# Kernel optimization log

Measured on AMD Instinct MI355X. Metric: run time of the kernel, lower is better.

## Reference

```python
import jax, jax.numpy as jnp
import numpy as np

STATE_DIM = 32
EMBED_DIM = 96
LATENT_DIM = STATE_DIM + EMBED_DIM  # 128
HISTORY = 8
HIST_DIM = HISTORY * STATE_DIM      # 256
CTRL_DIM = 8
HW = 512
BATCH = 4096
HORIZON = 64


def setup_inputs() -> dict:
    key = jax.random.key(0)
    ks = jax.random.split(key, 14)

    def w(k, shape, fan_in):
        return (jax.random.normal(k, shape, jnp.float32) / np.float32(np.sqrt(fan_in)))

    inp = {
        "history_k": jax.random.normal(ks[0], (BATCH, HIST_DIM), jnp.float32),
        "u_seq": jax.random.normal(ks[1], (BATCH, HORIZON, CTRL_DIM), jnp.float32),
        "history_next_seq": jax.random.normal(ks[2], (BATCH, HORIZON, HIST_DIM), jnp.float32),
        # encoder MLP: depth=3 -> 4 linear layers (256->512, 512->512, 512->512, 512->96)
        "enc_W0": w(ks[3], (HW, HIST_DIM), HIST_DIM),
        "enc_b0": jnp.zeros((HW,), jnp.float32),
        "enc_W1": w(ks[4], (HW, HW), HW),
        "enc_b1": jnp.zeros((HW,), jnp.float32),
        "enc_W2": w(ks[5], (HW, HW), HW),
        "enc_b2": jnp.zeros((HW,), jnp.float32),
        "enc_W3": w(ks[6], (EMBED_DIM, HW), HW),
        "enc_b3": jnp.zeros((EMBED_DIM,), jnp.float32),
        # A scaled so spectral radius ~0.9 (stable 64-step rollout)
        "A_W": jax.random.normal(ks[7], (LATENT_DIM, LATENT_DIM), jnp.float32) * np.float32(0.9 / np.sqrt(LATENT_DIM)),
        "B_W": w(ks[8], (LATENT_DIM, CTRL_DIM), CTRL_DIM),
    }
    return inp


def _encoder(x, W0, b0, W1, b1, W2, b2, W3, b3):
    h = jax.nn.relu(x @ W0.T + b0)
    h = jax.nn.relu(h @ W1.T + b1)
    h = jax.nn.relu(h @ W2.T + b2)
    return h @ W3.T + b3


def _lift(hist, W0, b0, W1, b1, W2, b2, W3, b3):
    cur = hist[..., -STATE_DIM:]
    return jnp.concatenate([cur, _encoder(hist, W0, b0, W1, b1, W2, b2, W3, b3)], axis=-1)


def reference(history_k, u_seq, history_next_seq,
              enc_W0, enc_b0, enc_W1, enc_b1, enc_W2, enc_b2, enc_W3, enc_b3,
              A_W, B_W):
    batch, horizon = u_seq.shape[:2]
    z_k = _lift(history_k, enc_W0, enc_b0, enc_W1, enc_b1, enc_W2, enc_b2, enc_W3, enc_b3)  # [B, L]

    hist_flat = history_next_seq.reshape(batch * horizon, HIST_DIM)
    z_target_seq = _lift(hist_flat, enc_W0, enc_b0, enc_W1, enc_b1, enc_W2, enc_b2, enc_W3, enc_b3)
    z_target_seq = z_target_seq.reshape(batch, horizon, LATENT_DIM)

    # Precompute B u_t for all steps: [M, B, L]
    bu = jnp.einsum('bmc,lc->mbl', u_seq, B_W)
    At = A_W.T

    def step(z, bu_t):
        z_next = z @ At + bu_t
        return z_next, z_next

    _, zs = jax.lax.scan(step, z_k, bu)          # zs: [M, B, L]
    z_pred_seq = jnp.swapaxes(zs, 0, 1)          # [B, M, L]
    x_pred_seq = z_pred_seq[..., :STATE_DIM]
    return (z_pred_seq, x_pred_seq, z_target_seq)
```

## Files before the change

kernel.cpp:

```cpp
#include <hip/hip_runtime.h>

#define XP_OFF 33554432L
#define ZT_OFF 41943040L

#define W0_OFF 0
#define W1_OFF 147456
#define W2_OFF 425984
#define W3_OFF 704512
#define ZK_BYTE_OFF 1513472L

typedef __attribute__((ext_vector_type(8))) short bf16x8;
typedef __attribute__((ext_vector_type(4))) float f32x4;

__device__ __forceinline__ unsigned short f2bf(float f){
  union { float ff; unsigned int uu; } c; c.ff = f;
  unsigned int u = c.uu;
  return (unsigned short)((u + 0x7FFFu + ((u >> 16) & 1u)) >> 16);
}

__global__ void cvt_kernel(const float* __restrict__ w0, const float* __restrict__ w1,
                           const float* __restrict__ w2, const float* __restrict__ w3,
                           unsigned short* __restrict__ o){
  int i = blockIdx.x * 256 + threadIdx.x;
  if (i < 131072){
    int r = i >> 8, c = i & 255;
    o[W0_OFF + r*288 + c] = f2bf(w0[i]);
  } else if (i < 393216){
    int j = i - 131072; int r = j >> 9, c = j & 511;
    o[W1_OFF + r*544 + c] = f2bf(w1[j]);
  } else if (i < 655360){
    int j = i - 393216; int r = j >> 9, c = j & 511;
    o[W2_OFF + r*544 + c] = f2bf(w2[j]);
  } else if (i < 704512){
    int j = i - 655360; int r = j >> 9, c = j & 511;
    o[W3_OFF + r*544 + c] = f2bf(w3[j]);
  }
}

template<int K, int WS, int NT, int MT>
__device__ __forceinline__ void gemm_tile(const unsigned short* __restrict__ W,
                                          const unsigned short* act,
                                          int lane, int ncol0, f32x4 (&acc)[NT][MT]){
  const int kl = (lane >> 4) << 3;
  const int ml = lane & 15;
  const unsigned short* wp = W + (ncol0 + ml)*WS + kl;
  bf16x8 bcur[NT], bnxt[NT];
#pragma unroll
  for (int nt = 0; nt < NT; ++nt)
    bcur[nt] = *(const bf16x8*)(wp + nt*16*WS);
#pragma unroll 1
  for (int kc = 0; kc < K/32; ++kc){
    if (kc + 1 < K/32){
#pragma unroll
      for (int nt = 0; nt < NT; ++nt)
        bnxt[nt] = *(const bf16x8*)(wp + nt*16*WS + (kc+1)*32);
    }
    const int kk = kc*32 + kl;
    bf16x8 a[MT];
#pragma unroll
    for (int mt = 0; mt < MT; ++mt){
      int m = mt*16 + ml;
      int byt = ((m << 10) + (kk << 1)) ^ ((m & 7) << 4);
      a[mt] = *(const bf16x8*)((const char*)act + byt);
    }
#pragma unroll
    for (int mt = 0; mt < MT; ++mt)
#pragma unroll
      for (int nt = 0; nt < NT; ++nt)
        acc[nt][mt] = __builtin_amdgcn_mfma_f32_16x16x32_bf16(bcur[nt], a[mt], acc[nt][mt], 0, 0, 0);
#pragma unroll
    for (int nt = 0; nt < NT; ++nt) bcur[nt] = bnxt[nt];
  }
}

template<int NT, int MT>
__device__ __forceinline__ void epi_lds(f32x4 (&acc)[NT][MT], const float* __restrict__ bias,
                                        int ncol0, int lane, unsigned short* act){
  const int ml = lane & 15;
  const int rl = (lane >> 4) << 2;
#pragma unroll
  for (int nt = 0; nt < NT; ++nt){
    int n0 = ncol0 + nt*16 + rl;
    float4 bn = *(const float4*)(bias + n0);
#pragma unroll
    for (int mt = 0; mt < MT; ++mt){
      int m = mt*16 + ml;
      float v0 = acc[nt][mt][0] + bn.x; v0 = v0 > 0.f ? v0 : 0.f;
      float v1 = acc[nt][mt][1] + bn.y; v1 = v1 > 0.f ? v1 : 0.f;
      float v2 = acc[nt][mt][2] + bn.z; v2 = v2 > 0.f ? v2 : 0.f;
      float v3 = acc[nt][mt][3] + bn.w; v3 = v3 > 0.f ? v3 : 0.f;
      ushort4 p; p.x = f2bf(v0); p.y = f2bf(v1); p.z = f2bf(v2); p.w = f2bf(v3);
      int byt = ((m << 10) + (n0 << 1)) ^ ((m & 7) << 4);
      *(ushort4*)((char*)act + byt) = p;
    }
  }
}

__global__ __launch_bounds__(256, 2) void enc_kernel(
    const float* __restrict__ histk, const float* __restrict__ histn,
    const unsigned short* __restrict__ wb,
    const float* __restrict__ b0, const float* __restrict__ b1,
    const float* __restrict__ b2, const float* __restrict__ b3,
    float* __restrict__ zk, float* __restrict__ out){
  __shared__ __align__(16) unsigned short act[64*512];
  const int tid  = threadIdx.x;
  const int lane = tid & 63;
  const int wave = tid >> 6;
  const int blk  = blockIdx.x;
  const bool is_zk = (blk < 64);
  const long r0 = (long)blk * 64;
  const float* __restrict__ src = is_zk ? (histk + r0*256) : (histn + (r0 - 4096)*256);
  const float4* src4 = (const float4*)src;

#pragma unroll 4
  for (int j = 0; j < 16; ++j){
    int vidx = j*256 + tid;
    float4 v = src4[vidx];
    int r  = vidx >> 6;
    int k0 = (vidx & 63) << 2;
    ushort4 p;
    p.x = f2bf(v.x); p.y = f2bf(v.y); p.z = f2bf(v.z); p.w = f2bf(v.w);
    int byt = ((r << 10) + (k0 << 1)) ^ ((r & 7) << 4);
    *(ushort4*)((char*)act + byt) = p;
    if (k0 >= 224){
      long rg = r0 + r;
      int c = k0 - 224;
      if (is_zk) *(float4*)(zk + rg*128 + c) = v;
      else       *(float4*)(out + ZT_OFF + (rg - 4096)*128 + c) = v;
    }
  }
  __syncthreads();

  {
    f32x4 acc[8][4];
#pragma unroll
    for (int i = 0; i < 8; ++i)
#pragma unroll
      for (int j = 0; j < 4; ++j) acc[i][j] = (f32x4){0.f,0.f,0.f,0.f};
    gemm_tile<256,288,8,4>(wb + W0_OFF, act, lane, wave*128, acc);
    __syncthreads();
    epi_lds<8,4>(acc, b0, wave*128, lane, act);
  }
  __syncthreads();
  {
    f32x4 acc[8][4];
#pragma unroll
    for (int i = 0; i < 8; ++i)
#pragma unroll
      for (int j = 0; j < 4; ++j) acc[i][j] = (f32x4){0.f,0.f,0.f,0.f};
    gemm_tile<512,544,8,4>(wb + W1_OFF, act, lane, wave*128, acc);
    __syncthreads();
    epi_lds<8,4>(acc, b1, wave*128, lane, act);
  }
  __syncthreads();
  {
    f32x4 acc[8][4];
#pragma unroll
    for (int i = 0; i < 8; ++i)
#pragma unroll
      for (int j = 0; j < 4; ++j) acc[i][j] = (f32x4){0.f,0.f,0.f,0.f};
    gemm_tile<512,544,8,4>(wb + W2_OFF, act, lane, wave*128, acc);
    __syncthreads();
    epi_lds<8,4>(acc, b2, wave*128, lane, act);
  }
  __syncthreads();
  {
    if (wave < 3){
      f32x4 acc[2][4];
#pragma unroll
      for (int i = 0; i < 2; ++i)
#pragma unroll
        for (int j = 0; j < 4; ++j) acc[i][j] = (f32x4){0.f,0.f,0.f,0.f};
      gemm_tile<512,544,2,4>(wb + W3_OFF, act, lane, wave*32, acc);
      const int ml = lane & 15, rl = (lane >> 4) << 2;
#pragma unroll
      for (int nt = 0; nt < 2; ++nt){
        int n0 = wave*32 + nt*16 + rl;
        float4 bn = *(const float4*)(b3 + n0);
#pragma unroll
        for (int mt = 0; mt < 4; ++mt){
          int m = mt*16 + ml;
          long rg = r0 + m;
          float4 v;
          v.x = acc[nt][mt][0] + bn.x;
          v.y = acc[nt][mt][1] + bn.y;
          v.z = acc[nt][mt][2] + bn.z;
          v.w = acc[nt][mt][3] + bn.w;
          if (is_zk) *(float4*)(zk + rg*128 + 32 + n0) = v;
          else       *(float4*)(out + ZT_OFF + (rg - 4096)*128 + 32 + n0) = v;
        }
      }
    }
  }
}

__global__ __launch_bounds__(256, 2) void scan_kernel(
    const float* __restrict__ A, const float* __restrict__ B,
    const float* __restrict__ u, const float* __restrict__ zkv,
    float* __restrict__ out){
  __shared__ __align__(16) float zbuf[2][2][128];
  __shared__ __align__(16) float ubuf[1024];
  const int tid = threadIdx.x;
  const int lr  = tid >> 7;
  const int l   = tid & 127;
  const long row = (long)blockIdx.x * 2 + lr;

  float Ar[128];
  const float4* A4 = (const float4*)A;
#pragma unroll
  for (int j4 = 0; j4 < 32; ++j4){
    float4 v = A4[l*32 + j4];
    Ar[4*j4] = v.x; Ar[4*j4+1] = v.y; Ar[4*j4+2] = v.z; Ar[4*j4+3] = v.w;
  }
  float Br[8];
  {
    const float4* B4 = (const float4*)B;
    float4 v0 = B4[l*2], v1 = B4[l*2+1];
    Br[0]=v0.x; Br[1]=v0.y; Br[2]=v0.z; Br[3]=v0.w;
    Br[4]=v1.x; Br[5]=v1.y; Br[6]=v1.z; Br[7]=v1.w;
  }
  ((float4*)ubuf)[tid] = ((const float4*)(u + (long)blockIdx.x*1024))[tid];
  zbuf[0][lr][l] = zkv[row*128 + l];
  __syncthreads();

  const long zp = row*8192 + l;
  const long xp = XP_OFF + row*2048 + l;
  int cur = 0;
#pragma unroll 1
  for (int t = 0; t < 64; ++t){
    const float* zc = zbuf[cur][lr];
    float acc = 0.f;
#pragma unroll
    for (int j4 = 0; j4 < 32; ++j4){
      float4 zv = ((const float4*)zc)[j4];
      acc += Ar[4*j4]*zv.x + Ar[4*j4+1]*zv.y + Ar[4*j4+2]*zv.z + Ar[4*j4+3]*zv.w;
    }
    const float4* uu = (const float4*)(ubuf + lr*512 + t*8);
    float4 u0 = uu[0], u1 = uu[1];
    acc += Br[0]*u0.x + Br[1]*u0.y + Br[2]*u0.z + Br[3]*u0.w
         + Br[4]*u1.x + Br[5]*u1.y + Br[6]*u1.z + Br[7]*u1.w;
    zbuf[cur^1][lr][l] = acc;
    out[zp + t*128] = acc;
    if (l < 32) out[xp + t*32] = acc;
    __syncthreads();
    cur ^= 1;
  }
}

extern "C" void kernel_launch(void* const* d_in, const int* in_sizes, int n_in,
                              void* d_out, int out_size, void* d_ws, size_t ws_size,
                              hipStream_t stream){
  const float* histk = (const float*)d_in[0];
  const float* useq  = (const float*)d_in[1];
  const float* histn = (const float*)d_in[2];
  const float* W0 = (const float*)d_in[3];
  const float* b0 = (const float*)d_in[4];
  const float* W1 = (const float*)d_in[5];
  const float* b1 = (const float*)d_in[6];
  const float* W2 = (const float*)d_in[7];
  const float* b2 = (const float*)d_in[8];
  const float* W3 = (const float*)d_in[9];
  const float* b3 = (const float*)d_in[10];
  const float* A  = (const float*)d_in[11];
  const float* B  = (const float*)d_in[12];
  float* out = (float*)d_out;

  unsigned short* wb = (unsigned short*)d_ws;
  float* zk = (float*)((char*)d_ws + ZK_BYTE_OFF);

  cvt_kernel <<<2752, 256, 0, stream>>>(W0, W1, W2, W3, wb);
  enc_kernel <<<4160, 256, 0, stream>>>(histk, histn, wb,
                                        b0, b1, b2, b3, zk, out);
  scan_kernel<<<2048, 256, 0, stream>>>(A, B, useq, zk, out);
}
```

Baseline: 749.6 us.

## Double encoder block row tile to 128 rows with 8 waves in 2x4 grid

```diff
diff --git a/kernel.cpp b/kernel.cpp
--- a/kernel.cpp
+++ b/kernel.cpp
@@ -40,7 +40,8 @@
 template<int K, int WS, int NT, int MT>
 __device__ __forceinline__ void gemm_tile(const unsigned short* __restrict__ W,
                                           const unsigned short* act,
-                                          int lane, int ncol0, f32x4 (&acc)[NT][MT]){
+                                          int lane, int nrow0, int ncol0,
+                                          f32x4 (&acc)[NT][MT]){
   const int kl = (lane >> 4) << 3;
   const int ml = lane & 15;
   const unsigned short* wp = W + (ncol0 + ml)*WS + kl;
@@ -59,7 +60,7 @@
     bf16x8 a[MT];
 #pragma unroll
     for (int mt = 0; mt < MT; ++mt){
-      int m = mt*16 + ml;
+      int m = nrow0 + mt*16 + ml;
       int byt = ((m << 10) + (kk << 1)) ^ ((m & 7) << 4);
       a[mt] = *(const bf16x8*)((const char*)act + byt);
     }
@@ -75,7 +76,7 @@
 
 template<int NT, int MT>
 __device__ __forceinline__ void epi_lds(f32x4 (&acc)[NT][MT], const float* __restrict__ bias,
-                                        int ncol0, int lane, unsigned short* act){
+                                        int nrow0, int ncol0, int lane, unsigned short* act){
   const int ml = lane & 15;
   const int rl = (lane >> 4) << 2;
 #pragma unroll
@@ -84,7 +85,7 @@
     float4 bn = *(const float4*)(bias + n0);
 #pragma unroll
     for (int mt = 0; mt < MT; ++mt){
-      int m = mt*16 + ml;
+      int m = nrow0 + mt*16 + ml;
       float v0 = acc[nt][mt][0] + bn.x; v0 = v0 > 0.f ? v0 : 0.f;
       float v1 = acc[nt][mt][1] + bn.y; v1 = v1 > 0.f ? v1 : 0.f;
       float v2 = acc[nt][mt][2] + bn.z; v2 = v2 > 0.f ? v2 : 0.f;
@@ -96,25 +97,27 @@
   }
 }
 
-__global__ __launch_bounds__(256, 2) void enc_kernel(
+__global__ __launch_bounds__(512, 2) void enc_kernel(
     const float* __restrict__ histk, const float* __restrict__ histn,
     const unsigned short* __restrict__ wb,
     const float* __restrict__ b0, const float* __restrict__ b1,
     const float* __restrict__ b2, const float* __restrict__ b3,
     float* __restrict__ zk, float* __restrict__ out){
-  __shared__ __align__(16) unsigned short act[64*512];
+  __shared__ __align__(16) unsigned short act[128*512];
   const int tid  = threadIdx.x;
   const int lane = tid & 63;
   const int wave = tid >> 6;
+  const int wr   = wave >> 2;
+  const int wc   = wave & 3;
   const int blk  = blockIdx.x;
-  const bool is_zk = (blk < 64);
-  const long r0 = (long)blk * 64;
+  const bool is_zk = (blk < 32);
+  const long r0 = (long)blk * 128;
   const float* __restrict__ src = is_zk ? (histk + r0*256) : (histn + (r0 - 4096)*256);
   const float4* src4 = (const float4*)src;
 
 #pragma unroll 4
   for (int j = 0; j < 16; ++j){
-    int vidx = j*256 + tid;
+    int vidx = j*512 + tid;
     float4 v = src4[vidx];
     int r  = vidx >> 6;
     int k0 = (vidx & 63) << 2;
@@ -137,9 +140,9 @@
     for (int i = 0; i < 8; ++i)
 #pragma unroll
       for (int j = 0; j < 4; ++j) acc[i][j] = (f32x4){0.f,0.f,0.f,0.f};
-    gemm_tile<256,288,8,4>(wb + W0_OFF, act, lane, wave*128, acc);
-    __syncthreads();
-    epi_lds<8,4>(acc, b0, wave*128, lane, act);
+    gemm_tile<256,288,8,4>(wb + W0_OFF, act, lane, wr*64, wc*128, acc);
+    __syncthreads();
+    epi_lds<8,4>(acc, b0, wr*64, wc*128, lane, act);
   }
   __syncthreads();
   {
@@ -148,9 +151,9 @@
     for (int i = 0; i < 8; ++i)
 #pragma unroll
       for (int j = 0; j < 4; ++j) acc[i][j] = (f32x4){0.f,0.f,0.f,0.f};
-    gemm_tile<512,544,8,4>(wb + W1_OFF, act, lane, wave*128, acc);
-    __syncthreads();
-    epi_lds<8,4>(acc, b1, wave*128, lane, act);
+    gemm_tile<512,544,8,4>(wb + W1_OFF, act, lane, wr*64, wc*128, acc);
+    __syncthreads();
+    epi_lds<8,4>(acc, b1, wr*64, wc*128, lane, act);
   }
   __syncthreads();
   {
@@ -159,27 +162,29 @@
     for (int i = 0; i < 8; ++i)
 #pragma unroll
       for (int j = 0; j < 4; ++j) acc[i][j] = (f32x4){0.f,0.f,0.f,0.f};
-    gemm_tile<512,544,8,4>(wb + W2_OFF, act, lane, wave*128, acc);
-    __syncthreads();
-    epi_lds<8,4>(acc, b2, wave*128, lane, act);
-  }
-  __syncthreads();
-  {
-    if (wave < 3){
+    gemm_tile<512,544,8,4>(wb + W2_OFF, act, lane, wr*64, wc*128, acc);
+    __syncthreads();
+    epi_lds<8,4>(acc, b2, wr*64, wc*128, lane, act);
+  }
+  __syncthreads();
+  {
+    if (wave < 6){
+      const int wr3 = wave & 1;
+      const int wc3 = wave >> 1;
       f32x4 acc[2][4];
 #pragma unroll
       for (int i = 0; i < 2; ++i)
 #pragma unroll
         for (int j = 0; j < 4; ++j) acc[i][j] = (f32x4){0.f,0.f,0.f,0.f};
-      gemm_tile<512,544,2,4>(wb + W3_OFF, act, lane, wave*32, acc);
+      gemm_tile<512,544,2,4>(wb + W3_OFF, act, lane, wr3*64, wc3*32, acc);
       const int ml = lane & 15, rl = (lane >> 4) << 2;
 #pragma unroll
       for (int nt = 0; nt < 2; ++nt){
-        int n0 = wave*32 + nt*16 + rl;
+        int n0 = wc3*32 + nt*16 + rl;
         float4 bn = *(const float4*)(b3 + n0);
 #pragma unroll
         for (int mt = 0; mt < 4; ++mt){
-          int m = mt*16 + ml;
+          int m = wr3*64 + mt*16 + ml;
           long rg = r0 + m;
           float4 v;
           v.x = acc[nt][mt][0] + bn.x;
@@ -269,7 +274,7 @@
   float* zk = (float*)((char*)d_ws + ZK_BYTE_OFF);
 
   cvt_kernel <<<2752, 256, 0, stream>>>(W0, W1, W2, W3, wb);
-  enc_kernel <<<4160, 256, 0, stream>>>(histk, histn, wb,
+  enc_kernel <<<2080, 512, 0, stream>>>(histk, histn, wb,
                                         b0, b1, b2, b3, zk, out);
   scan_kernel<<<2048, 256, 0, stream>>>(A, B, useq, zk, out);
 }
```

Measured after the change: 850.4 us. 13.4% more time.
